# Kernel tuning notes

Measured on AMD Instinct MI355X. Metric: run time of the kernel, lower is better.

The kernel has to match this reference:

```python
import jax, jax.numpy as jnp
import numpy as np
from jax import lax

B, CI, CO, H, W = 8, 64, 64, 256, 256
M1 = M2 = 16
RANK, NEXP, SCALING = 4, 15, 0.1
G = 4  # expert_region_size = sqrt(num_experts + 1)
WF = W // 2 + 1

# expert i occupies grid cell (row, col) = ((i+1)//G, (i+1)%G); cell (0,0) is the base weights1 corner
_IDX = np.arange(1, NEXP + 1)
RR = jnp.asarray(_IDX // G)
CC = jnp.asarray(_IDX % G)


def setup_inputs() -> dict:
    key = jax.random.key(0)
    ks = jax.random.split(key, 20)
    rn = lambda k, shape, s: jax.random.normal(k, shape, jnp.float32) * s
    scale = 1.0 / (CI * CO)
    return {
        "x": rn(ks[0], (B, CI, H, W), 1.0),
        "w1_re": jax.random.uniform(ks[1], (CI, CO, M1, M2), jnp.float32) * scale,
        "w1_im": jax.random.uniform(ks[2], (CI, CO, M1, M2), jnp.float32) * scale,
        "w2_re": jax.random.uniform(ks[3], (CI, CO, M1, M2), jnp.float32) * scale,
        "w2_im": jax.random.uniform(ks[4], (CI, CO, M1, M2), jnp.float32) * scale,
        "la1_re": rn(ks[5], (NEXP, RANK, CI), 0.02),
        "la1_im": rn(ks[6], (NEXP, RANK, CI), 0.02),
        "lb1_re": rn(ks[7], (NEXP, CO, RANK, M1, M2), 0.02),
        "lb1_im": rn(ks[8], (NEXP, CO, RANK, M1, M2), 0.02),
        "la2_re": rn(ks[9], (NEXP, RANK, CI), 0.02),
        "la2_im": rn(ks[10], (NEXP, RANK, CI), 0.02),
        "lb2_re": rn(ks[11], (NEXP, CO, RANK, M1, M2), 0.02),
        "lb2_im": rn(ks[12], (NEXP, CO, RANK, M1, M2), 0.02),
        "gate1": rn(ks[13], (NEXP,), 0.1),
        "gate2": rn(ks[14], (NEXP,), 0.1),
    }


def reference(x, w1_re, w1_im, w2_re, w2_im,
              la1_re, la1_im, lb1_re, lb1_im,
              la2_re, la2_im, lb2_re, lb2_im,
              gate1, gate2):
    x_ft = jnp.fft.rfft2(x)  # [B, CI, H, WF] complex64

    # scalar gates (gate_on_data=False): sigmoid(gate / temperature), temperature=1
    g1 = jax.nn.sigmoid(gate1)  # [E]
    g2 = jax.nn.sigmoid(gate2)
    sploss = jnp.mean(g1) + jnp.mean(g2)

    w1 = lax.complex(w1_re, w1_im)
    w2 = lax.complex(w2_re, w2_im)
    la1 = lax.complex(la1_re, la1_im)
    lb1 = lax.complex(lb1_re, lb1_im)
    la2 = lax.complex(la2_re, la2_im)
    lb2 = lax.complex(lb2_re, lb2_im)

    # per-expert LoRA weights: sum_r lora_b[o,r,x,y] * lora_a[r,i] -> [E, I, O, M1, M2]
    lw1 = jnp.einsum("eri,eorxy->eioxy", la1, lb1) * SCALING
    lw2 = jnp.einsum("eri,eorxy->eioxy", la2, lb2) * SCALING

    # base corner products
    top_base = jnp.einsum("bixy,ioxy->boxy", x_ft[:, :, :M1, :M2], w1)
    bot_base = jnp.einsum("bixy,ioxy->boxy", x_ft[:, :, H - M1:, :M2], w2)

    # gather all expert input tiles at once via a GxG grid view of the low-freq corners
    top = x_ft[:, :, :G * M1, :G * M2].reshape(B, CI, G, M1, G, M2)
    topt = jnp.transpose(top, (2, 4, 0, 1, 3, 5))        # [G, G, B, CI, M1, M2]
    xe1 = topt[RR, CC]                                    # [E, B, CI, M1, M2]
    bot = x_ft[:, :, H - G * M1:, :G * M2].reshape(B, CI, G, M1, G, M2)
    bott = jnp.transpose(bot, (2, 4, 0, 1, 3, 5))
    xe2 = bott[G - 1 - RR, CC]  # rows H-row_end:H-row_start == bottom-grid block 3-row_idx

    oe1 = jnp.einsum("ebixy,eioxy->eboxy", xe1, lw1) * g1[:, None, None, None, None]
    oe2 = jnp.einsum("ebixy,eioxy->eboxy", xe2, lw2) * g2[:, None, None, None, None]

    # scatter all disjoint tiles back into out_ft
    out_top = jnp.zeros((G, G, B, CO, M1, M2), jnp.complex64)
    out_top = out_top.at[0, 0].set(top_base).at[RR, CC].set(oe1)
    out_bot = jnp.zeros((G, G, B, CO, M1, M2), jnp.complex64)
    out_bot = out_bot.at[G - 1, 0].set(bot_base).at[G - 1 - RR, CC].set(oe2)

    out_ft = jnp.zeros((B, CO, H, WF), jnp.complex64)
    top_full = jnp.transpose(out_top, (2, 3, 0, 4, 1, 5)).reshape(B, CO, G * M1, G * M2)
    bot_full = jnp.transpose(out_bot, (2, 3, 0, 4, 1, 5)).reshape(B, CO, G * M1, G * M2)
    out_ft = out_ft.at[:, :, :G * M1, :G * M2].set(top_full)
    out_ft = out_ft.at[:, :, H - G * M1:, :G * M2].set(bot_full)

    y = jnp.fft.irfft2(out_ft, s=(H, W))
    return (y, sploss)
```

## Files before the change

kernel.cpp:

```cpp
#include <hip/hip_runtime.h>
#include <math.h>

#define B_   8
#define CI_  64
#define CO_  64
#define H_   256
#define W_   256
#define NE_  15
#define RK_  4

typedef __attribute__((ext_vector_type(8))) short short8;
typedef __attribute__((ext_vector_type(4))) float f32x4;

__device__ __forceinline__ unsigned bf16u(float f) {
  return (__float_as_uint(f) + 0x8000u) >> 16;
}
__device__ __forceinline__ unsigned pk2(float lo, float hi) {
  return ((__float_as_uint(lo) + 0x8000u) >> 16) |
         ((__float_as_uint(hi) + 0x8000u) & 0xFFFF0000u);
}
__device__ __forceinline__ float ubf(unsigned short u) {
  return __uint_as_float(((unsigned)u) << 16);
}

__global__ __launch_bounds__(256) void kTab(unsigned short* __restrict__ TAt,
                                            unsigned short* __restrict__ TB,
                                            unsigned short* __restrict__ TD,
                                            unsigned short* __restrict__ TEt) {
  int idx = blockIdx.x * 256 + threadIdx.x;
  const float C = 6.28318530717958647692f / 256.f;
  if (idx < 32768) {
    int n = idx >> 8, q = idx & 255;
    int w = n >> 1, pl = n & 1;
    int mm = (q * w) & 255;
    float s, c; sincosf(C * (float)mm, &s, &c);
    TAt[idx] = (unsigned short)bf16u(pl ? -s : c);
    return;
  }
  idx -= 32768;
  if (idx < 131072) {
    int mrow = idx >> 9, k = idx & 511;
    int p = k >> 1, tt = k & 1;
    int hr = mrow & 127, imr = mrow >> 7;
    int h = (hr < 64) ? hr : hr + 128;
    int mm = (p * h) & 255;
    float s, c; sincosf(C * (float)mm, &s, &c);
    float v = (imr == 0) ? (tt == 0 ? c : s) : (tt == 0 ? -s : c);
    TB[idx] = (unsigned short)bf16u(v);
    return;
  }
  idx -= 131072;
  if (idx < 131072) {
    int mrow = idx >> 8, k = idx & 255;
    int hr = k >> 1, tt = k & 1;
    int p = mrow & 255, imr = mrow >> 8;
    int h = (hr < 64) ? hr : hr + 128;
    int mm = (p * h) & 255;
    float s, c; sincosf(C * (float)mm, &s, &c);
    float v = (imr == 0) ? (tt == 0 ? c : -s) : (tt == 0 ? s : c);
    TD[idx] = (unsigned short)bf16u(v);
    return;
  }
  idx -= 131072;
  if (idx < 32768) {
    int q = idx >> 7, k = idx & 127;
    int w = k >> 1, pl = k & 1;
    int mm = (q * w) & 255;
    float s, c; sincosf(C * (float)mm, &s, &c);
    float v = (pl == 0) ? ((w == 0 ? 1.f : 2.f * c) / 65536.f)
                        : ((w == 0 ? 0.f : -2.f * s) / 65536.f);
    TEt[idx] = (unsigned short)bf16u(v);
  }
}

__global__ __launch_bounds__(256) void kGA(const float* __restrict__ x,
                                           const unsigned short* __restrict__ TAt,
                                           unsigned short* __restrict__ XcT) {
  __shared__ unsigned short As[128 * 32];
  __shared__ unsigned short Bs[128 * 32];
  __shared__ unsigned short Tt[64 * 264];
  int t = threadIdx.x;
  int lane = t & 63, wid = t >> 6;
  int row0 = blockIdx.x * 128;
  int mb = (wid >> 1) * 64, nb = (wid & 1) * 64;
  int lrow = lane & 15, lk = (lane >> 4) * 8;
  f32x4 acc[4][4];
#pragma unroll
  for (int a = 0; a < 4; ++a)
#pragma unroll
    for (int b = 0; b < 4; ++b) acc[a][b] = (f32x4){0.f, 0.f, 0.f, 0.f};

  for (int kk = 0; kk < 8; ++kk) {
    int k0 = kk * 32;
    __syncthreads();
    {
      int r = t >> 1, hf = t & 1;
      const float* xp = x + (size_t)(row0 + r) * 256 + k0 + hf * 16;
      float4 v0 = *(const float4*)(xp);
      float4 v1 = *(const float4*)(xp + 4);
      float4 v2 = *(const float4*)(xp + 8);
      float4 v3 = *(const float4*)(xp + 12);
      uint4 o0, o1;
      o0.x = pk2(v0.x, v0.y); o0.y = pk2(v0.z, v0.w);
      o0.z = pk2(v1.x, v1.y); o0.w = pk2(v1.z, v1.w);
      o1.x = pk2(v2.x, v2.y); o1.y = pk2(v2.z, v2.w);
      o1.z = pk2(v3.x, v3.y); o1.w = pk2(v3.z, v3.w);
      uint4* dst = (uint4*)&As[r * 32 + hf * 16];
      dst[0] = o0; dst[1] = o1;
    }
#pragma unroll
    for (int j = 0; j < 2; ++j) {
      int c = j * 256 + t;
      int n = c >> 2, seg = c & 3;
      *(uint4*)&Bs[n * 32 + seg * 8] = *(const uint4*)&TAt[n * 256 + k0 + seg * 8];
    }
    __syncthreads();
    short8 af[4], bf[4];
#pragma unroll
    for (int a = 0; a < 4; ++a)
      af[a] = *(const short8*)&As[(mb + a * 16 + lrow) * 32 + lk];
#pragma unroll
    for (int b = 0; b < 4; ++b)
      bf[b] = *(const short8*)&Bs[(nb + b * 16 + lrow) * 32 + lk];
#pragma unroll
    for (int a = 0; a < 4; ++a)
#pragma unroll
      for (int b = 0; b < 4; ++b)
        acc[a][b] = __builtin_amdgcn_mfma_f32_16x16x32_bf16(af[a], bf[b], acc[a][b], 0, 0, 0);
  }
#pragma unroll
  for (int a = 0; a < 4; ++a)
#pragma unroll
    for (int b = 0; b < 4; ++b)
#pragma unroll
      for (int r = 0; r < 4; ++r) {
        int m = mb + a * 16 + (lane >> 4) * 4 + r;
        int n = nb + b * 16 + lrow;
        Tt[(n >> 1) * 264 + 2 * m + (n & 1)] = (unsigned short)bf16u(acc[a][b][r]);
      }
  __syncthreads();
  {
    int bi = row0 >> 8;
    int p0 = row0 & 255;
    int w = t >> 2, seg = t & 3;
    unsigned short* dst = XcT + (size_t)bi * 32768 + w * 512 + p0 * 2 + seg * 64;
    const unsigned short* src = &Tt[w * 264 + seg * 64];
#pragma unroll
    for (int j = 0; j < 8; ++j)
      *(uint4*)(dst + j * 8) = *(const uint4*)(src + j * 8);
  }
}

__global__ __launch_bounds__(256) void kGB(const unsigned short* __restrict__ XcT,
                                           const unsigned short* __restrict__ TB,
                                           unsigned short* __restrict__ Xf) {
  __shared__ unsigned short As[256 * 32];
  __shared__ unsigned short Bs[64 * 32];
  int t = threadIdx.x, lane = t & 63, wid = t >> 6;
  int bi = blockIdx.x;
  const unsigned short* Xrow = XcT + (size_t)bi * 32768;
  int mb = wid * 64;
  int lrow = lane & 15, lk = (lane >> 4) * 8;
  f32x4 acc[4][4];
#pragma unroll
  for (int a = 0; a < 4; ++a)
#pragma unroll
    for (int b = 0; b < 4; ++b) acc[a][b] = (f32x4){0.f, 0.f, 0.f, 0.f};

  for (int kk = 0; kk < 16; ++kk) {
    int k0 = kk * 32;
    __syncthreads();
#pragma unroll
    for (int j = 0; j < 4; ++j) {
      int c = j * 256 + t;
      int m = c >> 2, seg = c & 3;
      *(uint4*)&As[m * 32 + seg * 8] = *(const uint4*)&TB[m * 512 + k0 + seg * 8];
    }
    {
      int n = t >> 2, seg = t & 3;
      *(uint4*)&Bs[n * 32 + seg * 8] = *(const uint4*)&Xrow[n * 512 + k0 + seg * 8];
    }
    __syncthreads();
    short8 af[4], bf[4];
#pragma unroll
    for (int a = 0; a < 4; ++a)
      af[a] = *(const short8*)&As[(mb + a * 16 + lrow) * 32 + lk];
#pragma unroll
    for (int b = 0; b < 4; ++b)
      bf[b] = *(const short8*)&Bs[(b * 16 + lrow) * 32 + lk];
#pragma unroll
    for (int a = 0; a < 4; ++a)
#pragma unroll
      for (int b = 0; b < 4; ++b)
        acc[a][b] = __builtin_amdgcn_mfma_f32_16x16x32_bf16(af[a], bf[b], acc[a][b], 0, 0, 0);
  }
  unsigned short* dst = Xf + (size_t)bi * 16384;
#pragma unroll
  for (int a = 0; a < 4; ++a)
#pragma unroll
    for (int b = 0; b < 4; ++b)
#pragma unroll
      for (int r = 0; r < 4; ++r) {
        int m = mb + a * 16 + (lane >> 4) * 4 + r;
        int n = b * 16 + lrow;
        dst[m * 64 + n] = (unsigned short)bf16u(acc[a][b][r]);
      }
}

__global__ __launch_bounds__(256) void kT(const unsigned short* __restrict__ Xf,
                                          float2* __restrict__ T,
                                          const float* __restrict__ la1re,
                                          const float* __restrict__ la1im,
                                          const float* __restrict__ la2re,
                                          const float* __restrict__ la2im) {
  int bid = blockIdx.x;
  int b = bid & 7;
  int e = (bid >> 3) % 15;
  int reg = bid / 120;
  int ep1 = e + 1;
  int grr = (reg == 0) ? (ep1 >> 2) : (3 - (ep1 >> 2));
  int gc = ep1 & 3;
  int hr0 = reg * 64 + grr * 16;
  int w0 = gc * 16;
  int t = threadIdx.x;
  int xx = t >> 4, yy = t & 15;
  const unsigned short* xp =
      Xf + (size_t)b * 64 * 16384 + (hr0 + xx) * 64 + (w0 + yy);
  const float* lare = (reg == 0) ? la1re : la2re;
  const float* laim = (reg == 0) ? la1im : la2im;
  float ar0 = 0.f, ai0 = 0.f, ar1 = 0.f, ai1 = 0.f;
  float ar2 = 0.f, ai2 = 0.f, ar3 = 0.f, ai3 = 0.f;
  for (int i = 0; i < 64; ++i) {
    float xr = ubf(xp[(size_t)i * 16384]);
    float xi = ubf(xp[(size_t)i * 16384 + 8192]);
    float l0r = lare[(e * 4 + 0) * 64 + i], l0i = laim[(e * 4 + 0) * 64 + i];
    float l1r = lare[(e * 4 + 1) * 64 + i], l1i = laim[(e * 4 + 1) * 64 + i];
    float l2r = lare[(e * 4 + 2) * 64 + i], l2i = laim[(e * 4 + 2) * 64 + i];
    float l3r = lare[(e * 4 + 3) * 64 + i], l3i = laim[(e * 4 + 3) * 64 + i];
    ar0 += l0r * xr - l0i * xi; ai0 += l0r * xi + l0i * xr;
    ar1 += l1r * xr - l1i * xi; ai1 += l1r * xi + l1i * xr;
    ar2 += l2r * xr - l2i * xi; ai2 += l2r * xi + l2i * xr;
    ar3 += l3r * xr - l3i * xi; ai3 += l3r * xi + l3i * xr;
  }
  float2* dst = T + ((((size_t)reg * 15 + e) * 8 + b) * 256 + t) * 4;
  dst[0] = make_float2(ar0, ai0);
  dst[1] = make_float2(ar1, ai1);
  dst[2] = make_float2(ar2, ai2);
  dst[3] = make_float2(ar3, ai3);
}

__global__ __launch_bounds__(256) void kD(const unsigned short* __restrict__ Xf,
                                          unsigned short* __restrict__ Gt,
                                          const float* __restrict__ w1re,
                                          const float* __restrict__ w1im,
                                          const float* __restrict__ w2re,
                                          const float* __restrict__ w2im) {
  __shared__ unsigned Xs[32 * 4 * 8 * 8];
  int bid = blockIdx.x;
  int yc = bid & 1, xc = (bid >> 1) & 3, oc = (bid >> 3) & 15, reg = bid >> 7;
  int hrb = (reg == 0) ? xc * 4 : 112 + xc * 4;
  const float* Wre = (reg == 0) ? w1re : w2re;
  const float* Wim = (reg == 0) ? w1im : w2im;
  int t = threadIdx.x;
  int b = t >> 5, o = (t >> 3) & 3, yy = t & 7;
  int og = oc * 4 + o, yyg = yc * 8 + yy;
  float ar[4] = {0.f, 0.f, 0.f, 0.f}, ai[4] = {0.f, 0.f, 0.f, 0.f};
  for (int ch = 0; ch < 2; ++ch) {
    __syncthreads();
#pragma unroll
    for (int j = 0; j < 4; ++j) {
      int seg = t + j * 256;
      int sb = seg >> 7, sx = (seg >> 5) & 3, si = seg & 31;
      int i = ch * 32 + si;
      const unsigned short* p =
          Xf + (size_t)(sb * 64 + i) * 16384 + (hrb + sx) * 64 + yc * 8;
      uint4 re = *(const uint4*)p;
      uint4 im = *(const uint4*)(p + 8192);
      uint4 o0, o1;
      o0.x = (re.x & 0xFFFFu) | (im.x << 16);
      o0.y = (re.x >> 16) | (im.x & 0xFFFF0000u);
      o0.z = (re.y & 0xFFFFu) | (im.y << 16);
      o0.w = (re.y >> 16) | (im.y & 0xFFFF0000u);
      o1.x = (re.z & 0xFFFFu) | (im.z << 16);
      o1.y = (re.z >> 16) | (im.z & 0xFFFF0000u);
      o1.z = (re.w & 0xFFFFu) | (im.w << 16);
      o1.w = (re.w >> 16) | (im.w & 0xFFFF0000u);
      uint4* d = (uint4*)&Xs[((si * 4 + sx) * 8 + sb) * 8];
      d[0] = o0; d[1] = o1;
    }
    __syncthreads();
    for (int ic = 0; ic < 32; ++ic) {
      int i = ch * 32 + ic;
#pragma unroll
      for (int xs = 0; xs < 4; ++xs) {
        unsigned pk = Xs[((ic * 4 + xs) * 8 + b) * 8 + yy];
        float xr = ubf((unsigned short)(pk & 0xFFFFu));
        float xi = ubf((unsigned short)(pk >> 16));
        int widx = ((i * 64 + og) * 16 + xc * 4 + xs) * 16 + yyg;
        float wr = Wre[widx], wi = Wim[widx];
        ar[xs] += xr * wr - xi * wi;
        ai[xs] += xr * wi + xi * wr;
      }
    }
  }
  uint4 ov;
  ov.x = pk2(ar[0], ai[0]);
  ov.y = pk2(ar[1], ai[1]);
  ov.z = pk2(ar[2], ai[2]);
  ov.w = pk2(ar[3], ai[3]);
  *(uint4*)(Gt + ((size_t)(b * 64 + og) * 64 + yyg) * 256 + 2 * hrb) = ov;
}

__global__ __launch_bounds__(256) void kM(const float2* __restrict__ T,
                                          unsigned short* __restrict__ Gt,
                                          const float* __restrict__ lb1re,
                                          const float* __restrict__ lb1im,
                                          const float* __restrict__ lb2re,
                                          const float* __restrict__ lb2im,
                                          const float* __restrict__ gate1,
                                          const float* __restrict__ gate2) {
  int bid = blockIdx.x;
  int hrc = bid & 7, oc = (bid >> 3) & 15, b = bid >> 7;
  int t = threadIdx.x;
  int w = t & 63, og = t >> 6;
  int o = oc * 4 + og;
  int reg = hrc >> 2;
  int grr = hrc & 3;
  int gc = w >> 4, yy = w & 15;
  int e = (reg == 0) ? (4 * grr + gc - 1) : (4 * (3 - grr) + gc - 1);
  if (e < 0) return;
  float gate = (reg == 0) ? gate1[e] : gate2[e];
  float g = 0.1f / (1.f + __expf(-gate));
  const float* lbre = (reg == 0) ? lb1re : lb2re;
  const float* lbim = (reg == 0) ? lb1im : lb2im;
  const float4* tp =
      (const float4*)(T + ((((size_t)reg * 15 + e) * 8 + b) * 256 + yy) * 4);
  size_t lbb = ((size_t)(e * 64 + o) * 4) * 256 + yy;
  unsigned out[16];
#pragma unroll
  for (int xx = 0; xx < 16; ++xx) {
    float4 t01 = tp[xx * 32];
    float4 t23 = tp[xx * 32 + 1];
    const float* pr = lbre + lbb + xx * 16;
    const float* pi = lbim + lbb + xx * 16;
    float b0r = pr[0],   b0i = pi[0];
    float b1r = pr[256], b1i = pi[256];
    float b2r = pr[512], b2i = pi[512];
    float b3r = pr[768], b3i = pi[768];
    float ar = 0.f, aim = 0.f;
    ar += t01.x * b0r - t01.y * b0i;  aim += t01.x * b0i + t01.y * b0r;
    ar += t01.z * b1r - t01.w * b1i;  aim += t01.z * b1i + t01.w * b1r;
    ar += t23.x * b2r - t23.y * b2i;  aim += t23.x * b2i + t23.y * b2r;
    ar += t23.z * b3r - t23.w * b3i;  aim += t23.z * b3i + t23.w * b3r;
    out[xx] = pk2(g * ar, g * aim);
  }
  uint4* dst = (uint4*)(Gt + ((size_t)(b * 64 + o) * 64 + w) * 256 + hrc * 32);
  dst[0] = make_uint4(out[0], out[1], out[2], out[3]);
  dst[1] = make_uint4(out[4], out[5], out[6], out[7]);
  dst[2] = make_uint4(out[8], out[9], out[10], out[11]);
  dst[3] = make_uint4(out[12], out[13], out[14], out[15]);
}

__global__ __launch_bounds__(512) void kGD(const unsigned short* __restrict__ Gt,
                                           const unsigned short* __restrict__ TD,
                                           unsigned short* __restrict__ Zt) {
  __shared__ unsigned short As[512 * 32];
  __shared__ unsigned short Bs[64 * 32];
  int t = threadIdx.x, lane = t & 63, wid = t >> 6;
  int bo = blockIdx.x;
  const unsigned short* Grow = Gt + (size_t)bo * 16384;
  int mb = wid * 64;
  int lrow = lane & 15, lk = (lane >> 4) * 8;
  f32x4 acc[4][4];
#pragma unroll
  for (int a = 0; a < 4; ++a)
#pragma unroll
    for (int b = 0; b < 4; ++b) acc[a][b] = (f32x4){0.f, 0.f, 0.f, 0.f};

  for (int kk = 0; kk < 8; ++kk) {
    int k0 = kk * 32;
    __syncthreads();
#pragma unroll
    for (int j = 0; j < 4; ++j) {
      int c = j * 512 + t;
      int m = c >> 2, seg = c & 3;
      *(uint4*)&As[m * 32 + seg * 8] = *(const uint4*)&TD[m * 256 + k0 + seg * 8];
    }
    if (t < 256) {
      int n = t >> 2, seg = t & 3;
      *(uint4*)&Bs[n * 32 + seg * 8] = *(const uint4*)&Grow[n * 256 + k0 + seg * 8];
    }
    __syncthreads();
    short8 af[4], bf[4];
#pragma unroll
    for (int a = 0; a < 4; ++a)
      af[a] = *(const short8*)&As[(mb + a * 16 + lrow) * 32 + lk];
#pragma unroll
    for (int b = 0; b < 4; ++b)
      bf[b] = *(const short8*)&Bs[(b * 16 + lrow) * 32 + lk];
#pragma unroll
    for (int a = 0; a < 4; ++a)
#pragma unroll
      for (int b = 0; b < 4; ++b)
        acc[a][b] = __builtin_amdgcn_mfma_f32_16x16x32_bf16(af[a], bf[b], acc[a][b], 0, 0, 0);
  }
  unsigned short* dst = Zt + (size_t)bo * 32768;
#pragma unroll
  for (int a = 0; a < 4; ++a)
#pragma unroll
    for (int b = 0; b < 4; ++b)
#pragma unroll
      for (int r = 0; r < 4; ++r) {
        int m = mb + a * 16 + (lane >> 4) * 4 + r;
        int p = m & 255, pl = m >> 8;
        int n = b * 16 + lrow;
        dst[p * 128 + 2 * n + pl] = (unsigned short)bf16u(acc[a][b][r]);
      }
}

__global__ __launch_bounds__(512) void kGE(const unsigned short* __restrict__ Zt,
                                           const unsigned short* __restrict__ TEt,
                                           float* __restrict__ y) {
  __shared__ unsigned short As[256 * 32];
  __shared__ unsigned short Bs[128 * 32];
  int t = threadIdx.x, lane = t & 63, wid = t >> 6;
  int bo = blockIdx.x >> 1, qh = blockIdx.x & 1;
  const unsigned short* Zrow = Zt + (size_t)bo * 32768;
  int mb = (wid >> 1) * 64, nb = (wid & 1) * 64;
  int lrow = lane & 15, lk = (lane >> 4) * 8;
  f32x4 acc[4][4];
#pragma unroll
  for (int a = 0; a < 4; ++a)
#pragma unroll
    for (int b = 0; b < 4; ++b) acc[a][b] = (f32x4){0.f, 0.f, 0.f, 0.f};

  for (int kk = 0; kk < 4; ++kk) {
    int k0 = kk * 32;
    __syncthreads();
#pragma unroll
    for (int j = 0; j < 2; ++j) {
      int c = j * 512 + t;
      int m = c >> 2, seg = c & 3;
      *(uint4*)&As[m * 32 + seg * 8] = *(const uint4*)&Zrow[m * 128 + k0 + seg * 8];
    }
    {
      int n = t >> 2, seg = t & 3;
      *(uint4*)&Bs[n * 32 + seg * 8] =
          *(const uint4*)&TEt[(qh * 128 + n) * 128 + k0 + seg * 8];
    }
    __syncthreads();
    short8 af[4], bf[4];
#pragma unroll
    for (int a = 0; a < 4; ++a)
      af[a] = *(const short8*)&As[(mb + a * 16 + lrow) * 32 + lk];
#pragma unroll
    for (int b = 0; b < 4; ++b)
      bf[b] = *(const short8*)&Bs[(nb + b * 16 + lrow) * 32 + lk];
#pragma unroll
    for (int a = 0; a < 4; ++a)
#pragma unroll
      for (int b = 0; b < 4; ++b)
        acc[a][b] = __builtin_amdgcn_mfma_f32_16x16x32_bf16(af[a], bf[b], acc[a][b], 0, 0, 0);
  }
  float* dst = y + (size_t)bo * 65536 + qh * 128;
#pragma unroll
  for (int a = 0; a < 4; ++a)
#pragma unroll
    for (int b = 0; b < 4; ++b)
#pragma unroll
      for (int r = 0; r < 4; ++r) {
        int p = mb + a * 16 + (lane >> 4) * 4 + r;
        int q = nb + b * 16 + lrow;
        dst[(size_t)p * 256 + q] = acc[a][b][r];
      }
}

__global__ void kS2(const float* __restrict__ gate1, const float* __restrict__ gate2,
                    float* __restrict__ out) {
  if (threadIdx.x == 0) {
    float s = 0.f;
    for (int e = 0; e < NE_; ++e)
      s += 1.f / (1.f + expf(-gate1[e])) + 1.f / (1.f + expf(-gate2[e]));
    out[0] = s / (float)NE_;
  }
}

extern "C" void kernel_launch(void* const* d_in, const int* in_sizes, int n_in,
                              void* d_out, int out_size, void* d_ws, size_t ws_size,
                              hipStream_t stream) {
  const float* x     = (const float*)d_in[0];
  const float* w1re  = (const float*)d_in[1];
  const float* w1im  = (const float*)d_in[2];
  const float* w2re  = (const float*)d_in[3];
  const float* w2im  = (const float*)d_in[4];
  const float* la1re = (const float*)d_in[5];
  const float* la1im = (const float*)d_in[6];
  const float* lb1re = (const float*)d_in[7];
  const float* lb1im = (const float*)d_in[8];
  const float* la2re = (const float*)d_in[9];
  const float* la2im = (const float*)d_in[10];
  const float* lb2re = (const float*)d_in[11];
  const float* lb2im = (const float*)d_in[12];
  const float* gate1 = (const float*)d_in[13];
  const float* gate2 = (const float*)d_in[14];

  char* ws = (char*)d_ws;
  unsigned short* XcT = (unsigned short*)ws;
  unsigned short* Xf  = (unsigned short*)(ws + ((size_t)32 << 20));
  unsigned short* Gt  = (unsigned short*)(ws + ((size_t)48 << 20));
  unsigned short* Zt  = (unsigned short*)(ws + ((size_t)64 << 20));
  unsigned short* TAt = (unsigned short*)(ws + ((size_t)96 << 20));
  unsigned short* TB  = TAt + 32768;
  unsigned short* TD  = TB + 131072;
  unsigned short* TEt = TD + 131072;
  float2* Tw = (float2*)(ws + ((size_t)97 << 20));
  float* y = (float*)d_out;

  kTab<<<1280, 256, 0, stream>>>(TAt, TB, TD, TEt);
  kGA<<<1024, 256, 0, stream>>>(x, TAt, XcT);
  kGB<<<512, 256, 0, stream>>>(XcT, TB, Xf);
  kT<<<240, 256, 0, stream>>>(Xf, Tw, la1re, la1im, la2re, la2im);
  kD<<<256, 256, 0, stream>>>(Xf, Gt, w1re, w1im, w2re, w2im);
  kM<<<1024, 256, 0, stream>>>(Tw, Gt, lb1re, lb1im, lb2re, lb2im, gate1, gate2);
  kGD<<<512, 512, 0, stream>>>(Gt, TD, Zt);
  kGE<<<1024, 512, 0, stream>>>(Zt, TEt, y);
  kS2<<<1, 64, 0, stream>>>(gate1, gate2, y + (size_t)B_ * CO_ * H_ * W_);
}
```

Before: 418.7 us.

## Fuse forward DFT stages into one kernel and restructure LoRA kM reuse

Merges the two forward-transform GEMM kernels (kGA, kGB) into a single kAB kernel. It keeps the intermediate column-DFT result in shared memory instead of round-tripping it through a global XcT buffer, which removes one launch and the intermediate global writes and reads. Separately, kM is regridded so each block loads its lora_b coefficients into registers once and loops over the batch, cutting redundant lora_b global reads. The trade-offs are higher LDS use per block in kAB, fewer kM blocks, and a serialized two-half loop inside each kAB block.

```diff
diff --git a/kernel.cpp b/kernel.cpp
--- a/kernel.cpp
+++ b/kernel.cpp
@@ -73,137 +73,109 @@
   }
 }
 
-__global__ __launch_bounds__(256) void kGA(const float* __restrict__ x,
-                                           const unsigned short* __restrict__ TAt,
-                                           unsigned short* __restrict__ XcT) {
-  __shared__ unsigned short As[128 * 32];
-  __shared__ unsigned short Bs[128 * 32];
-  __shared__ unsigned short Tt[64 * 264];
-  int t = threadIdx.x;
-  int lane = t & 63, wid = t >> 6;
-  int row0 = blockIdx.x * 128;
-  int mb = (wid >> 1) * 64, nb = (wid & 1) * 64;
-  int lrow = lane & 15, lk = (lane >> 4) * 8;
-  f32x4 acc[4][4];
-#pragma unroll
-  for (int a = 0; a < 4; ++a)
-#pragma unroll
-    for (int b = 0; b < 4; ++b) acc[a][b] = (f32x4){0.f, 0.f, 0.f, 0.f};
-
-  for (int kk = 0; kk < 8; ++kk) {
-    int k0 = kk * 32;
-    __syncthreads();
-    {
-      int r = t >> 1, hf = t & 1;
-      const float* xp = x + (size_t)(row0 + r) * 256 + k0 + hf * 16;
-      float4 v0 = *(const float4*)(xp);
-      float4 v1 = *(const float4*)(xp + 4);
-      float4 v2 = *(const float4*)(xp + 8);
-      float4 v3 = *(const float4*)(xp + 12);
-      uint4 o0, o1;
-      o0.x = pk2(v0.x, v0.y); o0.y = pk2(v0.z, v0.w);
-      o0.z = pk2(v1.x, v1.y); o0.w = pk2(v1.z, v1.w);
-      o1.x = pk2(v2.x, v2.y); o1.y = pk2(v2.z, v2.w);
-      o1.z = pk2(v3.x, v3.y); o1.w = pk2(v3.z, v3.w);
-      uint4* dst = (uint4*)&As[r * 32 + hf * 16];
-      dst[0] = o0; dst[1] = o1;
-    }
-#pragma unroll
-    for (int j = 0; j < 2; ++j) {
-      int c = j * 256 + t;
-      int n = c >> 2, seg = c & 3;
-      *(uint4*)&Bs[n * 32 + seg * 8] = *(const uint4*)&TAt[n * 256 + k0 + seg * 8];
-    }
-    __syncthreads();
-    short8 af[4], bf[4];
-#pragma unroll
-    for (int a = 0; a < 4; ++a)
-      af[a] = *(const short8*)&As[(mb + a * 16 + lrow) * 32 + lk];
-#pragma unroll
-    for (int b = 0; b < 4; ++b)
-      bf[b] = *(const short8*)&Bs[(nb + b * 16 + lrow) * 32 + lk];
-#pragma unroll
-    for (int a = 0; a < 4; ++a)
-#pragma unroll
-      for (int b = 0; b < 4; ++b)
-        acc[a][b] = __builtin_amdgcn_mfma_f32_16x16x32_bf16(af[a], bf[b], acc[a][b], 0, 0, 0);
-  }
-#pragma unroll
-  for (int a = 0; a < 4; ++a)
-#pragma unroll
-    for (int b = 0; b < 4; ++b)
-#pragma unroll
-      for (int r = 0; r < 4; ++r) {
-        int m = mb + a * 16 + (lane >> 4) * 4 + r;
-        int n = nb + b * 16 + lrow;
-        Tt[(n >> 1) * 264 + 2 * m + (n & 1)] = (unsigned short)bf16u(acc[a][b][r]);
-      }
-  __syncthreads();
-  {
-    int bi = row0 >> 8;
-    int p0 = row0 & 255;
-    int w = t >> 2, seg = t & 3;
-    unsigned short* dst = XcT + (size_t)bi * 32768 + w * 512 + p0 * 2 + seg * 64;
-    const unsigned short* src = &Tt[w * 264 + seg * 64];
-#pragma unroll
-    for (int j = 0; j < 8; ++j)
-      *(uint4*)(dst + j * 8) = *(const uint4*)(src + j * 8);
-  }
-}
-
-__global__ __launch_bounds__(256) void kGB(const unsigned short* __restrict__ XcT,
-                                           const unsigned short* __restrict__ TB,
-                                           unsigned short* __restrict__ Xf) {
+__global__ __launch_bounds__(512, 4) void kAB(const float* __restrict__ x,
+                                              const unsigned short* __restrict__ TAt,
+                                              const unsigned short* __restrict__ TB,
+                                              unsigned short* __restrict__ Xf) {
   __shared__ unsigned short As[256 * 32];
-  __shared__ unsigned short Bs[64 * 32];
+  __shared__ unsigned short Bs1[128 * 32];
+  __shared__ unsigned short XcL[64 * 264];
   int t = threadIdx.x, lane = t & 63, wid = t >> 6;
   int bi = blockIdx.x;
-  const unsigned short* Xrow = XcT + (size_t)bi * 32768;
-  int mb = wid * 64;
+  const float* xb = x + (size_t)bi * 65536;
   int lrow = lane & 15, lk = (lane >> 4) * 8;
-  f32x4 acc[4][4];
-#pragma unroll
-  for (int a = 0; a < 4; ++a)
-#pragma unroll
-    for (int b = 0; b < 4; ++b) acc[a][b] = (f32x4){0.f, 0.f, 0.f, 0.f};
-
-  for (int kk = 0; kk < 16; ++kk) {
-    int k0 = kk * 32;
-    __syncthreads();
-#pragma unroll
-    for (int j = 0; j < 4; ++j) {
-      int c = j * 256 + t;
-      int m = c >> 2, seg = c & 3;
-      *(uint4*)&As[m * 32 + seg * 8] = *(const uint4*)&TB[m * 512 + k0 + seg * 8];
-    }
-    {
-      int n = t >> 2, seg = t & 3;
-      *(uint4*)&Bs[n * 32 + seg * 8] = *(const uint4*)&Xrow[n * 512 + k0 + seg * 8];
-    }
-    __syncthreads();
-    short8 af[4], bf[4];
-#pragma unroll
-    for (int a = 0; a < 4; ++a)
-      af[a] = *(const short8*)&As[(mb + a * 16 + lrow) * 32 + lk];
+  f32x4 acc2[2][4];
+#pragma unroll
+  for (int a = 0; a < 2; ++a)
+#pragma unroll
+    for (int b = 0; b < 4; ++b) acc2[a][b] = (f32x4){0.f, 0.f, 0.f, 0.f};
+
+  for (int half = 0; half < 2; ++half) {
+    f32x4 acc1[2][4];
+#pragma unroll
+    for (int a = 0; a < 2; ++a)
+#pragma unroll
+      for (int b = 0; b < 4; ++b) acc1[a][b] = (f32x4){0.f, 0.f, 0.f, 0.f};
+    int mb1 = (wid >> 1) * 32, nb1 = (wid & 1) * 64;
+    for (int kk = 0; kk < 8; ++kk) {
+      int k0 = kk * 32;
+      __syncthreads();
+      {
+        int r = t >> 2, hf = t & 3;
+        const float* xp = xb + (size_t)(half * 128 + r) * 256 + k0 + hf * 8;
+        float4 v0 = *(const float4*)(xp);
+        float4 v1 = *(const float4*)(xp + 4);
+        uint4 o;
+        o.x = pk2(v0.x, v0.y); o.y = pk2(v0.z, v0.w);
+        o.z = pk2(v1.x, v1.y); o.w = pk2(v1.z, v1.w);
+        *(uint4*)&As[r * 32 + hf * 8] = o;
+      }
+      {
+        int n = t >> 2, seg = t & 3;
+        *(uint4*)&Bs1[n * 32 + seg * 8] = *(const uint4*)&TAt[n * 256 + k0 + seg * 8];
+      }
+      __syncthreads();
+      short8 af[2], bf[4];
+#pragma unroll
+      for (int a = 0; a < 2; ++a)
+        af[a] = *(const short8*)&As[(mb1 + a * 16 + lrow) * 32 + lk];
+#pragma unroll
+      for (int b = 0; b < 4; ++b)
+        bf[b] = *(const short8*)&Bs1[(nb1 + b * 16 + lrow) * 32 + lk];
+#pragma unroll
+      for (int a = 0; a < 2; ++a)
+#pragma unroll
+        for (int b = 0; b < 4; ++b)
+          acc1[a][b] = __builtin_amdgcn_mfma_f32_16x16x32_bf16(af[a], bf[b], acc1[a][b], 0, 0, 0);
+    }
+    __syncthreads();
+#pragma unroll
+    for (int a = 0; a < 2; ++a)
+#pragma unroll
+      for (int b = 0; b < 4; ++b)
+#pragma unroll
+        for (int r = 0; r < 4; ++r) {
+          int m = mb1 + a * 16 + (lane >> 4) * 4 + r;
+          int n = nb1 + b * 16 + lrow;
+          XcL[(n >> 1) * 264 + 2 * m + (n & 1)] = (unsigned short)bf16u(acc1[a][b][r]);
+        }
+    __syncthreads();
+    int mb2 = wid * 32;
+    for (int kk = 0; kk < 8; ++kk) {
+      int k0 = kk * 32;
+      __syncthreads();
+#pragma unroll
+      for (int j = 0; j < 2; ++j) {
+        int c = j * 512 + t;
+        int m = c >> 2, seg = c & 3;
+        *(uint4*)&As[m * 32 + seg * 8] =
+            *(const uint4*)&TB[m * 512 + half * 256 + k0 + seg * 8];
+      }
+      __syncthreads();
+      short8 af2[2], bf2[4];
+#pragma unroll
+      for (int a = 0; a < 2; ++a)
+        af2[a] = *(const short8*)&As[(mb2 + a * 16 + lrow) * 32 + lk];
+#pragma unroll
+      for (int b = 0; b < 4; ++b)
+        bf2[b] = *(const short8*)&XcL[(b * 16 + lrow) * 264 + k0 + lk];
+#pragma unroll
+      for (int a = 0; a < 2; ++a)
+#pragma unroll
+        for (int b = 0; b < 4; ++b)
+          acc2[a][b] = __builtin_amdgcn_mfma_f32_16x16x32_bf16(af2[a], bf2[b], acc2[a][b], 0, 0, 0);
+    }
+  }
+  unsigned short* dst = Xf + (size_t)bi * 16384;
+#pragma unroll
+  for (int a = 0; a < 2; ++a)
 #pragma unroll
     for (int b = 0; b < 4; ++b)
-      bf[b] = *(const short8*)&Bs[(b * 16 + lrow) * 32 + lk];
-#pragma unroll
-    for (int a = 0; a < 4; ++a)
-#pragma unroll
-      for (int b = 0; b < 4; ++b)
-        acc[a][b] = __builtin_amdgcn_mfma_f32_16x16x32_bf16(af[a], bf[b], acc[a][b], 0, 0, 0);
-  }
-  unsigned short* dst = Xf + (size_t)bi * 16384;
-#pragma unroll
-  for (int a = 0; a < 4; ++a)
-#pragma unroll
-    for (int b = 0; b < 4; ++b)
 #pragma unroll
       for (int r = 0; r < 4; ++r) {
-        int m = mb + a * 16 + (lane >> 4) * 4 + r;
+        int m = wid * 32 + a * 16 + (lane >> 4) * 4 + r;
         int n = b * 16 + lrow;
-        dst[m * 64 + n] = (unsigned short)bf16u(acc[a][b][r]);
+        dst[m * 64 + n] = (unsigned short)bf16u(acc2[a][b][r]);
       }
 }
 
@@ -320,7 +292,7 @@
                                           const float* __restrict__ gate1,
                                           const float* __restrict__ gate2) {
   int bid = blockIdx.x;
-  int hrc = bid & 7, oc = (bid >> 3) & 15, b = bid >> 7;
+  int xc = bid & 3, hrc = (bid >> 2) & 7, oc = bid >> 5;
   int t = threadIdx.x;
   int w = t & 63, og = t >> 6;
   int o = oc * 4 + og;
@@ -333,32 +305,42 @@
   float g = 0.1f / (1.f + __expf(-gate));
   const float* lbre = (reg == 0) ? lb1re : lb2re;
   const float* lbim = (reg == 0) ? lb1im : lb2im;
-  const float4* tp =
-      (const float4*)(T + ((((size_t)reg * 15 + e) * 8 + b) * 256 + yy) * 4);
   size_t lbb = ((size_t)(e * 64 + o) * 4) * 256 + yy;
-  unsigned out[16];
-#pragma unroll
-  for (int xx = 0; xx < 16; ++xx) {
-    float4 t01 = tp[xx * 32];
-    float4 t23 = tp[xx * 32 + 1];
+  float blr[4][4], bli[4][4];
+#pragma unroll
+  for (int x2 = 0; x2 < 4; ++x2) {
+    int xx = xc * 4 + x2;
     const float* pr = lbre + lbb + xx * 16;
     const float* pi = lbim + lbb + xx * 16;
-    float b0r = pr[0],   b0i = pi[0];
-    float b1r = pr[256], b1i = pi[256];
-    float b2r = pr[512], b2i = pi[512];
-    float b3r = pr[768], b3i = pi[768];
-    float ar = 0.f, aim = 0.f;
-    ar += t01.x * b0r - t01.y * b0i;  aim += t01.x * b0i + t01.y * b0r;
-    ar += t01.z * b1r - t01.w * b1i;  aim += t01.z * b1i + t01.w * b1r;
-    ar += t23.x * b2r - t23.y * b2i;  aim += t23.x * b2i + t23.y * b2r;
-    ar += t23.z * b3r - t23.w * b3i;  aim += t23.z * b3i + t23.w * b3r;
-    out[xx] = pk2(g * ar, g * aim);
-  }
-  uint4* dst = (uint4*)(Gt + ((size_t)(b * 64 + o) * 64 + w) * 256 + hrc * 32);
-  dst[0] = make_uint4(out[0], out[1], out[2], out[3]);
-  dst[1] = make_uint4(out[4], out[5], out[6], out[7]);
-  dst[2] = make_uint4(out[8], out[9], out[10], out[11]);
-  dst[3] = make_uint4(out[12], out[13], out[14], out[15]);
+#pragma unroll
+    for (int r = 0; r < 4; ++r) {
+      blr[x2][r] = pr[r * 256];
+      bli[x2][r] = pi[r * 256];
+    }
+  }
+  const size_t tbase = (((size_t)reg * 15 + e) * 8) * 256 + yy;
+  for (int b = 0; b < 8; ++b) {
+    const float4* tp = (const float4*)(T + (tbase + (size_t)b * 256) * 4);
+    unsigned out4[4];
+#pragma unroll
+    for (int x2 = 0; x2 < 4; ++x2) {
+      int xx = xc * 4 + x2;
+      float4 t01 = tp[xx * 32];
+      float4 t23 = tp[xx * 32 + 1];
+      float ar = 0.f, aim = 0.f;
+      ar += t01.x * blr[x2][0] - t01.y * bli[x2][0];
+      aim += t01.x * bli[x2][0] + t01.y * blr[x2][0];
+      ar += t01.z * blr[x2][1] - t01.w * bli[x2][1];
+      aim += t01.z * bli[x2][1] + t01.w * blr[x2][1];
+      ar += t23.x * blr[x2][2] - t23.y * bli[x2][2];
+      aim += t23.x * bli[x2][2] + t23.y * blr[x2][2];
+      ar += t23.z * blr[x2][3] - t23.w * bli[x2][3];
+      aim += t23.z * bli[x2][3] + t23.w * blr[x2][3];
+      out4[x2] = pk2(g * ar, g * aim);
+    }
+    *(uint4*)(Gt + ((size_t)(b * 64 + o) * 64 + w) * 256 + hrc * 32 + xc * 8) =
+        make_uint4(out4[0], out4[1], out4[2], out4[3]);
+  }
 }
 
 __global__ __launch_bounds__(512) void kGD(const unsigned short* __restrict__ Gt,
@@ -505,7 +487,6 @@
   const float* gate2 = (const float*)d_in[14];
 
   char* ws = (char*)d_ws;
-  unsigned short* XcT = (unsigned short*)ws;
   unsigned short* Xf  = (unsigned short*)(ws + ((size_t)32 << 20));
   unsigned short* Gt  = (unsigned short*)(ws + ((size_t)48 << 20));
   unsigned short* Zt  = (unsigned short*)(ws + ((size_t)64 << 20));
@@ -517,11 +498,10 @@
   float* y = (float*)d_out;
 
   kTab<<<1280, 256, 0, stream>>>(TAt, TB, TD, TEt);
-  kGA<<<1024, 256, 0, stream>>>(x, TAt, XcT);
-  kGB<<<512, 256, 0, stream>>>(XcT, TB, Xf);
+  kAB<<<512, 512, 0, stream>>>(x, TAt, TB, Xf);
   kT<<<240, 256, 0, stream>>>(Xf, Tw, la1re, la1im, la2re, la2im);
   kD<<<256, 256, 0, stream>>>(Xf, Gt, w1re, w1im, w2re, w2im);
-  kM<<<1024, 256, 0, stream>>>(Tw, Gt, lb1re, lb1im, lb2re, lb2im, gate1, gate2);
+  kM<<<512, 256, 0, stream>>>(Tw, Gt, lb1re, lb1im, lb2re, lb2im, gate1, gate2);
   kGD<<<512, 512, 0, stream>>>(Gt, TD, Zt);
   kGE<<<1024, 512, 0, stream>>>(Zt, TEt, y);
   kS2<<<1, 64, 0, stream>>>(gate1, gate2, y + (size_t)B_ * CO_ * H_ * W_);
```

Measured after the change: 406.6 us. 2.9% less time.
